# Kernel tuning notes

Hardware: AMD Instinct MI355X
Metric: run time of the kernel (lower is better)

Reference implementation:

```python
import jax, jax.numpy as jnp
import numpy as np

N, DIM, H, D = 8192, 1152, 16, 72
SEGS = 4  # equal-length image segments


def setup_inputs() -> dict:
    key = jax.random.key(0)
    ks = jax.random.split(key, 8)
    s = 0.02
    return {
        "hidden_states": jax.random.normal(ks[0], (N, DIM), jnp.float32),
        "cos": jax.random.uniform(ks[1], (N, D), jnp.float32, -1.0, 1.0),
        "sin": jax.random.uniform(ks[2], (N, D), jnp.float32, -1.0, 1.0),
        "cu_seqlens": (jnp.arange(SEGS + 1, dtype=jnp.int32) * (N // SEGS)),
        "w_qkv": jax.random.normal(ks[3], (DIM, 3 * DIM), jnp.float32) * s,
        "b_qkv": jax.random.normal(ks[4], (3 * DIM,), jnp.float32) * s,
        "w_proj": jax.random.normal(ks[5], (DIM, DIM), jnp.float32) * s,
        "b_proj": jax.random.normal(ks[6], (DIM,), jnp.float32) * s,
    }


def _rope(x, cos, sin):
    # x: [N, H, D]; cos/sin: [N, 1, D]
    half = x.shape[-1] // 2
    x1, x2 = x[..., :half], x[..., half:]
    rot = jnp.concatenate([-x2, x1], axis=-1)
    return x * cos + rot * sin


def reference(hidden_states, cos, sin, cu_seqlens, w_qkv, b_qkv, w_proj, b_proj):
    n = hidden_states.shape[0]
    qkv = (hidden_states @ w_qkv + b_qkv).reshape(n, 3, H, D)
    q, k, v = qkv[:, 0], qkv[:, 1], qkv[:, 2]
    c = cos[:, None, :]
    s = sin[:, None, :]
    q = _rope(q, c, s)
    k = _rope(k, c, s)
    # equal-length segments derived statically from cu_seqlens
    segs = int(cu_seqlens.shape[0]) - 1
    L = n // segs
    qs = q.reshape(segs, L, H, D)
    ks = k.reshape(segs, L, H, D)
    vs = v.reshape(segs, L, H, D)
    scale = D ** -0.5
    scores = jnp.einsum("slhd,smhd->shlm", qs, ks) * scale
    attn = jax.nn.softmax(scores, axis=-1)
    out = jnp.einsum("shlm,smhd->slhd", attn, vs).reshape(n, DIM)
    return out @ w_proj + b_proj
```

## Files before the change

### kernel.cpp

```cpp
#include <hip/hip_runtime.h>
#include <hip/hip_bf16.h>
#include <cstdint>
#include <cstddef>

typedef __bf16 bf16;
typedef __attribute__((ext_vector_type(8))) __bf16 bf16x8;
typedef __attribute__((ext_vector_type(4))) float f32x4;
typedef __attribute__((ext_vector_type(16))) float f32x16;
typedef __attribute__((ext_vector_type(4))) float floatx4;
typedef __attribute__((ext_vector_type(4))) unsigned short ushort4_t;
typedef __attribute__((ext_vector_type(2))) unsigned uint2_t;
typedef __attribute__((ext_vector_type(4))) unsigned uint4_t;

#define NTOK 8192
#define DIMM 1152
#define NH   16
#define HD   72
#define SEGS 4
#define SEGL 2048

__device__ __forceinline__ void gload16(const void* gsrc, void* ldst) {
  __builtin_amdgcn_global_load_lds(
      (const __attribute__((address_space(1))) void*)gsrc,
      (__attribute__((address_space(3))) void*)ldst,
      16, 0, 0);
}

__device__ __forceinline__ unsigned cvtpk(float a, float b) {
  unsigned r;
  asm volatile("v_cvt_pk_bf16_f32 %0, %1, %2" : "=v"(r) : "v"(a), "v"(b));
  return r;
}

__global__ __launch_bounds__(256) void k_cvt(const float* __restrict__ src,
                                             bf16* __restrict__ dst, int n8) {
  int i = blockIdx.x * 256 + threadIdx.x;
  if (i >= n8) return;
  const floatx4* s = (const floatx4*)src + (size_t)i * 2;
  floatx4 a = s[0], b = s[1];
  uint4_t o;
  o[0] = cvtpk(a.x, a.y);
  o[1] = cvtpk(a.z, a.w);
  o[2] = cvtpk(b.x, b.y);
  o[3] = cvtpk(b.z, b.w);
  *((uint4_t*)dst + i) = o;
}

__global__ __launch_bounds__(256) void k_twt(const float* __restrict__ src,
                                             bf16* __restrict__ dst, int R, int C) {
  __shared__ bf16 tile[64][73];
  int bc = blockIdx.x * 64, br = blockIdx.y * 64;
  int t = threadIdx.x;
#pragma unroll
  for (int i = 0; i < 16; i++) {
    int idx = i * 256 + t;
    int r = idx >> 6, c = idx & 63;
    float v = (bc + c < C) ? src[(size_t)(br + r) * C + bc + c] : 0.f;
    tile[c][r] = (bf16)v;
  }
  __syncthreads();
#pragma unroll
  for (int i = 0; i < 16; i++) {
    int idx = i * 256 + t;
    int r = idx >> 6, c = idx & 63;
    dst[(size_t)(bc + r) * R + br + c] = tile[r][c];
  }
}

template <int BM, int BN, int MI, int NI, int THREADS, bool OUT_F32>
__global__ __launch_bounds__(THREADS, 2) void k_gemmP(const bf16* __restrict__ A,
                                                      const bf16* __restrict__ Bt,
                                                      const float* __restrict__ bias,
                                                      void* __restrict__ Cout,
                                                      int M, int Nreal, int K, int gx) {
  __shared__ bf16 sA[3][BM * 32];
  __shared__ bf16 sB[3][BN * 32];
  constexpr int WN = BN / (NI * 16);
  constexpr int nA = (BM * 4) / THREADS;
  constexpr int nB = (BN * 4) / THREADS;
  constexpr int NLD = nA + nB;
  static_assert(NLD == 3 || NLD == 4, "vmcnt literal");
  const int t = threadIdx.x, wave = t >> 6, lane = t & 63;
  const int lr = lane & 15, lg = lane >> 4;
  const int nwg = gridDim.x, bid = blockIdx.x;
  const int swz = (bid & 7) * (nwg >> 3) + (bid >> 3);
  const int bx = swz % gx, by = swz / gx;
  const int m0 = by * BM, n0 = bx * BN;
  const int wr = wave / WN, wc = wave % WN;
  const int NS = K >> 5;

  f32x4 acc[MI][NI];
#pragma unroll
  for (int i = 0; i < MI; i++)
#pragma unroll
    for (int j = 0; j < NI; j++)
#pragma unroll
      for (int q = 0; q < 4; q++) acc[i][j][q] = 0.f;

  const bf16* Ab = A + (size_t)m0 * K;
  const bf16* Bb = Bt + (size_t)n0 * K;
  const int glsw = ((t & 3) ^ ((t >> 3) & 3)) * 8;
  const int rbase = t >> 2;

  auto STAGE = [&](int slot, int k0) {
#pragma unroll
    for (int p = 0; p < nA; ++p)
      gload16(Ab + (size_t)(rbase + p * (THREADS / 4)) * K + k0 + glsw,
              (char*)&sA[slot][0] + p * (THREADS * 16) + wave * 1024);
#pragma unroll
    for (int p = 0; p < nB; ++p)
      gload16(Bb + (size_t)(rbase + p * (THREADS / 4)) * K + k0 + glsw,
              (char*)&sB[slot][0] + p * (THREADS * 16) + wave * 1024);
  };

  const int swz4 = (lr >> 1) & 3;
  const int aoff = (wr * MI * 16 + lr) * 32 + ((lg ^ swz4) * 8);
  const int boff = (wc * NI * 16 + lr) * 32 + ((lg ^ swz4) * 8);

  STAGE(0, 0);
  STAGE(1, 32);

  int slot = 0;
  for (int j = 0; j < NS; ++j) {
    if (j == NS - 1) {
      asm volatile("s_waitcnt vmcnt(0)" ::: "memory");
    } else if constexpr (NLD == 3) {
      asm volatile("s_waitcnt vmcnt(3)" ::: "memory");
    } else {
      asm volatile("s_waitcnt vmcnt(4)" ::: "memory");
    }
    __builtin_amdgcn_s_barrier();
    __builtin_amdgcn_sched_barrier(0);
    bf16x8 av[MI], bv[NI];
#pragma unroll
    for (int mi = 0; mi < MI; mi++)
      av[mi] = *(const bf16x8*)&sA[slot][aoff + mi * 512];
#pragma unroll
    for (int ni = 0; ni < NI; ni++)
      bv[ni] = *(const bf16x8*)&sB[slot][boff + ni * 512];
    asm volatile("s_waitcnt lgkmcnt(0)" ::: "memory");
    __builtin_amdgcn_sched_barrier(0);
    if (j + 2 < NS) {
      int s2 = slot + 2; if (s2 >= 3) s2 -= 3;
      STAGE(s2, (j + 2) * 32);
    }
    __builtin_amdgcn_s_setprio(1);
#pragma unroll
    for (int mi = 0; mi < MI; mi++)
#pragma unroll
      for (int ni = 0; ni < NI; ni++)
        acc[mi][ni] = __builtin_amdgcn_mfma_f32_16x16x32_bf16(av[mi], bv[ni], acc[mi][ni], 0, 0, 0);
    __builtin_amdgcn_s_setprio(0);
    if (++slot == 3) slot = 0;
  }

#pragma unroll
  for (int mi = 0; mi < MI; ++mi)
#pragma unroll
    for (int ni = 0; ni < NI; ++ni) {
      int col = n0 + wc * NI * 16 + ni * 16 + lr;
      if (col < Nreal) {
        float bc_ = bias[col];
#pragma unroll
        for (int j = 0; j < 4; j++) {
          int row = m0 + wr * MI * 16 + mi * 16 + lg * 4 + j;
          float v = acc[mi][ni][j] + bc_;
          if (OUT_F32)
            ((float*)Cout)[(size_t)row * Nreal + col] = v;
          else
            ((bf16*)Cout)[(size_t)row * Nreal + col] = (bf16)v;
        }
      }
    }
}

__global__ __launch_bounds__(256) void k_rope(const bf16* __restrict__ qkv,
                                              const float* __restrict__ cs,
                                              const float* __restrict__ sn,
                                              bf16* __restrict__ Qp,
                                              bf16* __restrict__ Kp) {
  int n = blockIdx.x;
  int s = n >> 11, l = n & 2047;
  const bf16* row = qkv + (size_t)n * (3 * DIMM);
  const float* cr = cs + (size_t)n * HD;
  const float* sr = sn + (size_t)n * HD;
  const float QS = 0.17002323f;
  for (int e = threadIdx.x; e < 3072; e += 256) {
    int which = e / 1536;
    int r = e - which * 1536;
    int h = r / 96;
    int d = r - h * 96;
    float v = 0.f;
    if (d < HD) {
      int base = which * DIMM + h * HD;
      float x = (float)row[base + d];
      float o = (d < 36) ? -(float)row[base + d + 36] : (float)row[base + d - 36];
      v = x * cr[d] + o * sr[d];
      if (which == 0) v *= QS;
    }
    bf16* dst = which ? Kp : Qp;
    dst[(((size_t)(s * NH + h) * 3 + (d >> 5)) * SEGL + l) * 32 + (d & 31)] = (bf16)v;
  }
}

__global__ __launch_bounds__(256) void k_vrep(const bf16* __restrict__ qkv,
                                              bf16* __restrict__ Vt) {
  int s = blockIdx.z, h = blockIdx.y, l0 = blockIdx.x * 64;
  __shared__ bf16 tl[64][73];
  int t = threadIdx.x;
  for (int idx = t; idx < 64 * HD; idx += 256) {
    int l = idx / HD, d = idx - l * HD;
    tl[l][d] = qkv[(size_t)(s * SEGL + l0 + l) * (3 * DIMM) + 2 * DIMM + h * HD + d];
  }
  __syncthreads();
  for (int idx = t; idx < 96 * 64; idx += 256) {
    int d = idx >> 6, l = idx & 63;
    bf16 v = (d < HD) ? tl[l][d] : ((d == HD) ? (bf16)1.f : (bf16)0.f);
    Vt[((size_t)(s * NH + h) * 96 + d) * SEGL + l0 + l] = v;
  }
}

__global__ __launch_bounds__(256, 2) void k_attn(const bf16* __restrict__ Qg,
                                                 const bf16* __restrict__ Kg,
                                                 const bf16* __restrict__ Vg,
                                                 bf16* __restrict__ Oo) {
  __shared__ bf16 sK[2][3 * 64 * 32];
  __shared__ bf16 sV[2][96 * 64];
  const int t = threadIdx.x, wave = t >> 6, lane = t & 63;
  const int c = lane & 31, hi = lane >> 5;
  const int bid = blockIdx.x;
  const int g = ((bid >> 6) << 3) | (bid & 7);
  const int qt = (bid >> 3) & 7;
  const int s = g >> 4, h = g & 15, q0 = qt * 256;
  const bf16* Qb = Qg + (size_t)(s * NH + h) * 3 * SEGL * 32;
  const bf16* Kb = Kg + (size_t)(s * NH + h) * 3 * SEGL * 32;
  const bf16* Vb = Vg + (size_t)(s * NH + h) * 96 * SEGL;

  const bf16* kq[3];
  const bf16* vq[3];
#pragma unroll
  for (int i = 0; i < 3; i++) {
    int ch = wave * 3 + i;
    int kk = ch >> 2;
    int r = (ch & 3) * 16 + (lane >> 2);
    int gg = (lane & 3) ^ ((r >> 1) & 3);
    kq[i] = Kb + (size_t)kk * (SEGL * 32) + (size_t)r * 32 + gg * 8;
    int rv = ch * 8 + (lane >> 3);
    int gv = (lane & 7) ^ (rv & 7);
    vq[i] = Vb + (size_t)rv * SEGL + gv * 8;
  }

  bf16x8 Qf[2][5];
#pragma unroll
  for (int sni = 0; sni < 2; sni++)
#pragma unroll
    for (int kk = 0; kk < 5; kk++) {
      int qr = q0 + wave * 64 + sni * 32 + c;
      Qf[sni][kk] = *(const bf16x8*)&Qb[(size_t)(kk >> 1) * (SEGL * 32) +
                                        (size_t)qr * 32 + ((kk & 1) * 2 + hi) * 8];
    }

#pragma unroll
  for (int i = 0; i < 3; i++) {
    gload16(kq[i], (char*)sK[0] + (wave * 3 + i) * 1024);
    gload16(vq[i], (char*)sV[0] + (wave * 3 + i) * 1024);
    kq[i] += 2048;
    vq[i] += 64;
  }
  __syncthreads();

  f32x16 accO[3][2];
#pragma unroll
  for (int df = 0; df < 3; df++)
#pragma unroll
    for (int sni = 0; sni < 2; sni++)
#pragma unroll
      for (int r = 0; r < 16; r++) accO[df][sni][r] = 0.f;
  f32x16 ZC;
#pragma unroll
  for (int r = 0; r < 16; r++) ZC[r] = 0.f;

  int cur = 0;
  for (int tile = 0; tile < 32; ++tile) {
    if (tile + 1 < 32) {
#pragma unroll
      for (int i = 0; i < 3; i++) {
        gload16(kq[i], (char*)sK[cur ^ 1] + (wave * 3 + i) * 1024);
        gload16(vq[i], (char*)sV[cur ^ 1] + (wave * 3 + i) * 1024);
        kq[i] += 2048;
        vq[i] += 64;
      }
    }

    f32x16 S[2][2];
    __builtin_amdgcn_s_setprio(1);
#pragma unroll
    for (int kk = 0; kk < 5; kk++) {
      bf16x8 Kf[2];
#pragma unroll
      for (int smi = 0; smi < 2; smi++) {
        int kr = smi * 32 + c;
        int gg = (((kk & 1) * 2 + hi) ^ ((kr >> 1) & 3));
        Kf[smi] = *(const bf16x8*)&sK[cur][(kk >> 1) * 2048 + kr * 32 + gg * 8];
      }
#pragma unroll
      for (int smi = 0; smi < 2; smi++)
#pragma unroll
        for (int sni = 0; sni < 2; sni++)
          S[smi][sni] = __builtin_amdgcn_mfma_f32_32x32x16_bf16(
              Kf[smi], Qf[sni][kk], kk ? S[smi][sni] : ZC, 0, 0, 0);
    }
    __builtin_amdgcn_s_setprio(0);

    __builtin_amdgcn_s_setprio(1);
#pragma unroll
    for (int kk = 0; kk < 4; kk++) {
      bf16x8 Vf[3];
#pragma unroll
      for (int df = 0; df < 3; df++) {
        int dr = df * 32 + c;
        int gg = ((kk * 2 + hi) ^ (dr & 7));
        Vf[df] = *(const bf16x8*)&sV[cur][dr * 64 + gg * 8];
      }
#pragma unroll
      for (int sni = 0; sni < 2; sni++) {
        const int smi = kk >> 1;
        const int base = (kk & 1) * 8;
        unsigned u0 = cvtpk(__builtin_amdgcn_exp2f(S[smi][sni][base + 0]),
                            __builtin_amdgcn_exp2f(S[smi][sni][base + 1]));
        unsigned u1 = cvtpk(__builtin_amdgcn_exp2f(S[smi][sni][base + 2]),
                            __builtin_amdgcn_exp2f(S[smi][sni][base + 3]));
        unsigned u2 = cvtpk(__builtin_amdgcn_exp2f(S[smi][sni][base + 4]),
                            __builtin_amdgcn_exp2f(S[smi][sni][base + 5]));
        unsigned u3 = cvtpk(__builtin_amdgcn_exp2f(S[smi][sni][base + 6]),
                            __builtin_amdgcn_exp2f(S[smi][sni][base + 7]));
        asm volatile("v_permlane32_swap_b32 %0, %1" : "+v"(u0), "+v"(u2));
        asm volatile("v_permlane32_swap_b32 %0, %1" : "+v"(u1), "+v"(u3));
        union { bf16x8 v; unsigned u[4]; } pb;
        pb.u[0] = u0; pb.u[1] = u1; pb.u[2] = u2; pb.u[3] = u3;
#pragma unroll
        for (int df = 0; df < 3; df++)
          accO[df][sni] = __builtin_amdgcn_mfma_f32_32x32x16_bf16(Vf[df], pb.v, accO[df][sni], 0, 0, 0);
      }
    }
    __builtin_amdgcn_s_setprio(0);

    __syncthreads();
    cur ^= 1;
  }

#pragma unroll
  for (int sni = 0; sni < 2; sni++) {
    float lown = accO[2][sni][4];
    float lv = lown + __shfl_xor(lown, 32, 64);
    float inv = 1.f / lv;
    int token = s * SEGL + q0 + wave * 64 + sni * 32 + c;
#pragma unroll
    for (int df = 0; df < 3; df++)
#pragma unroll
      for (int rg = 0; rg < 4; rg++) {
        int d0 = df * 32 + rg * 8 + hi * 4;
        if (d0 < HD) {
          uint2_t w;
          w[0] = cvtpk(accO[df][sni][rg * 4 + 0] * inv, accO[df][sni][rg * 4 + 1] * inv);
          w[1] = cvtpk(accO[df][sni][rg * 4 + 2] * inv, accO[df][sni][rg * 4 + 3] * inv);
          *(uint2_t*)&Oo[(size_t)token * DIMM + h * HD + d0] = w;
        }
      }
  }
}

extern "C" void kernel_launch(void* const* d_in, const int* in_sizes, int n_in,
                              void* d_out, int out_size, void* d_ws, size_t ws_size,
                              hipStream_t stream) {
  (void)in_sizes; (void)n_in; (void)out_size; (void)ws_size;
  const float* hs     = (const float*)d_in[0];
  const float* cosp   = (const float*)d_in[1];
  const float* sinp   = (const float*)d_in[2];
  const float* w_qkv  = (const float*)d_in[4];
  const float* b_qkv  = (const float*)d_in[5];
  const float* w_proj = (const float*)d_in[6];
  const float* b_proj = (const float*)d_in[7];
  float* out = (float*)d_out;

  char* ws = (char*)d_ws;
  bf16* hsb    = (bf16*)(ws + 0);
  bf16* wprojT = (bf16*)(ws + 26836992);
  bf16* qkv    = (bf16*)(ws + 29491200);
  bf16* Qp     = (bf16*)(ws + 86114304);
  bf16* Kp     = (bf16*)(ws + 111280128);
  bf16* Vt     = (bf16*)(ws + 136445952);
  bf16* ao     = (bf16*)(ws + 161611776);
  bf16* wqkvT  = (bf16*)(ws + 161611776);

  k_cvt<<<4608, 256, 0, stream>>>(hs, hsb, 1179648);
  k_twt<<<dim3(56, 18), 256, 0, stream>>>(w_qkv, wqkvT, 1152, 3456);
  k_twt<<<dim3(18, 18), 256, 0, stream>>>(w_proj, wprojT, 1152, 1152);
  k_gemmP<128, 256, 4, 4, 512, false><<<896, 512, 0, stream>>>(
      hsb, wqkvT, b_qkv, (void*)qkv, 8192, 3456, 1152, 14);
  k_rope<<<8192, 256, 0, stream>>>(qkv, cosp, sinp, Qp, Kp);
  k_vrep<<<dim3(32, 16, 4), 256, 0, stream>>>(qkv, Vt);
  k_attn<<<512, 256, 0, stream>>>(Qp, Kp, Vt, ao);
  k_gemmP<128, 128, 4, 4, 256, true><<<576, 256, 0, stream>>>(
      ao, wprojT, b_proj, (void*)out, 8192, 1152, 1152, 9);
}
```

Measured before the change: 289.8 us.

## Halve attention query tile and shrink QKV GEMM tile for more occupancy

```diff
diff --git a/kernel.cpp b/kernel.cpp
--- a/kernel.cpp
+++ b/kernel.cpp
@@ -8,7 +8,6 @@
 typedef __attribute__((ext_vector_type(4))) float f32x4;
 typedef __attribute__((ext_vector_type(16))) float f32x16;
 typedef __attribute__((ext_vector_type(4))) float floatx4;
-typedef __attribute__((ext_vector_type(4))) unsigned short ushort4_t;
 typedef __attribute__((ext_vector_type(2))) unsigned uint2_t;
 typedef __attribute__((ext_vector_type(4))) unsigned uint4_t;
 
@@ -68,7 +67,7 @@
 }
 
 template <int BM, int BN, int MI, int NI, int THREADS, bool OUT_F32>
-__global__ __launch_bounds__(THREADS, 2) void k_gemmP(const bf16* __restrict__ A,
+__global__ __launch_bounds__(THREADS, 3) void k_gemmP(const bf16* __restrict__ A,
                                                       const bf16* __restrict__ Bt,
                                                       const float* __restrict__ bias,
                                                       void* __restrict__ Cout,
@@ -220,7 +219,7 @@
   }
 }
 
-__global__ __launch_bounds__(256, 2) void k_attn(const bf16* __restrict__ Qg,
+__global__ __launch_bounds__(256, 3) void k_attn(const bf16* __restrict__ Qg,
                                                  const bf16* __restrict__ Kg,
                                                  const bf16* __restrict__ Vg,
                                                  bf16* __restrict__ Oo) {
@@ -229,9 +228,9 @@
   const int t = threadIdx.x, wave = t >> 6, lane = t & 63;
   const int c = lane & 31, hi = lane >> 5;
   const int bid = blockIdx.x;
-  const int g = ((bid >> 6) << 3) | (bid & 7);
-  const int qt = (bid >> 3) & 7;
-  const int s = g >> 4, h = g & 15, q0 = qt * 256;
+  const int g = ((bid >> 7) << 3) | (bid & 7);
+  const int qt = (bid >> 3) & 15;
+  const int s = g >> 4, h = g & 15, q0 = qt * 128;
   const bf16* Qb = Qg + (size_t)(s * NH + h) * 3 * SEGL * 32;
   const bf16* Kb = Kg + (size_t)(s * NH + h) * 3 * SEGL * 32;
   const bf16* Vb = Vg + (size_t)(s * NH + h) * 96 * SEGL;
@@ -250,15 +249,13 @@
     vq[i] = Vb + (size_t)rv * SEGL + gv * 8;
   }
 
-  bf16x8 Qf[2][5];
-#pragma unroll
-  for (int sni = 0; sni < 2; sni++)
-#pragma unroll
-    for (int kk = 0; kk < 5; kk++) {
-      int qr = q0 + wave * 64 + sni * 32 + c;
-      Qf[sni][kk] = *(const bf16x8*)&Qb[(size_t)(kk >> 1) * (SEGL * 32) +
-                                        (size_t)qr * 32 + ((kk & 1) * 2 + hi) * 8];
-    }
+  bf16x8 Qf[5];
+#pragma unroll
+  for (int kk = 0; kk < 5; kk++) {
+    int qr = q0 + wave * 32 + c;
+    Qf[kk] = *(const bf16x8*)&Qb[(size_t)(kk >> 1) * (SEGL * 32) +
+                                 (size_t)qr * 32 + ((kk & 1) * 2 + hi) * 8];
+  }
 
 #pragma unroll
   for (int i = 0; i < 3; i++) {
@@ -269,13 +266,11 @@
   }
   __syncthreads();
 
-  f32x16 accO[3][2];
+  f32x16 accO[3];
 #pragma unroll
   for (int df = 0; df < 3; df++)
 #pragma unroll
-    for (int sni = 0; sni < 2; sni++)
-#pragma unroll
-      for (int r = 0; r < 16; r++) accO[df][sni][r] = 0.f;
+    for (int r = 0; r < 16; r++) accO[df][r] = 0.f;
   f32x16 ZC;
 #pragma unroll
   for (int r = 0; r < 16; r++) ZC[r] = 0.f;
@@ -292,7 +287,7 @@
       }
     }
 
-    f32x16 S[2][2];
+    f32x16 S[2];
     __builtin_amdgcn_s_setprio(1);
 #pragma unroll
     for (int kk = 0; kk < 5; kk++) {
@@ -305,10 +300,8 @@
       }
 #pragma unroll
       for (int smi = 0; smi < 2; smi++)
-#pragma unroll
-        for (int sni = 0; sni < 2; sni++)
-          S[smi][sni] = __builtin_amdgcn_mfma_f32_32x32x16_bf16(
-              Kf[smi], Qf[sni][kk], kk ? S[smi][sni] : ZC, 0, 0, 0);
+        S[smi] = __builtin_amdgcn_mfma_f32_32x32x16_bf16(
+            Kf[smi], Qf[kk], kk ? S[smi] : ZC, 0, 0, 0);
     }
     __builtin_amdgcn_s_setprio(0);
 
@@ -322,26 +315,23 @@
         int gg = ((kk * 2 + hi) ^ (dr & 7));
         Vf[df] = *(const bf16x8*)&sV[cur][dr * 64 + gg * 8];
       }
-#pragma unroll
-      for (int sni = 0; sni < 2; sni++) {
-        const int smi = kk >> 1;
-        const int base = (kk & 1) * 8;
-        unsigned u0 = cvtpk(__builtin_amdgcn_exp2f(S[smi][sni][base + 0]),
-                            __builtin_amdgcn_exp2f(S[smi][sni][base + 1]));
-        unsigned u1 = cvtpk(__builtin_amdgcn_exp2f(S[smi][sni][base + 2]),
-                            __builtin_amdgcn_exp2f(S[smi][sni][base + 3]));
-        unsigned u2 = cvtpk(__builtin_amdgcn_exp2f(S[smi][sni][base + 4]),
-                            __builtin_amdgcn_exp2f(S[smi][sni][base + 5]));
-        unsigned u3 = cvtpk(__builtin_amdgcn_exp2f(S[smi][sni][base + 6]),
-                            __builtin_amdgcn_exp2f(S[smi][sni][base + 7]));
-        asm volatile("v_permlane32_swap_b32 %0, %1" : "+v"(u0), "+v"(u2));
-        asm volatile("v_permlane32_swap_b32 %0, %1" : "+v"(u1), "+v"(u3));
-        union { bf16x8 v; unsigned u[4]; } pb;
-        pb.u[0] = u0; pb.u[1] = u1; pb.u[2] = u2; pb.u[3] = u3;
-#pragma unroll
-        for (int df = 0; df < 3; df++)
-          accO[df][sni] = __builtin_amdgcn_mfma_f32_32x32x16_bf16(Vf[df], pb.v, accO[df][sni], 0, 0, 0);
-      }
+      const int smi = kk >> 1;
+      const int base = (kk & 1) * 8;
+      unsigned u0 = cvtpk(__builtin_amdgcn_exp2f(S[smi][base + 0]),
+                          __builtin_amdgcn_exp2f(S[smi][base + 1]));
+      unsigned u1 = cvtpk(__builtin_amdgcn_exp2f(S[smi][base + 2]),
+                          __builtin_amdgcn_exp2f(S[smi][base + 3]));
+      unsigned u2 = cvtpk(__builtin_amdgcn_exp2f(S[smi][base + 4]),
+                          __builtin_amdgcn_exp2f(S[smi][base + 5]));
+      unsigned u3 = cvtpk(__builtin_amdgcn_exp2f(S[smi][base + 6]),
+                          __builtin_amdgcn_exp2f(S[smi][base + 7]));
+      asm volatile("v_permlane32_swap_b32 %0, %1" : "+v"(u0), "+v"(u2));
+      asm volatile("v_permlane32_swap_b32 %0, %1" : "+v"(u1), "+v"(u3));
+      union { bf16x8 v; unsigned u[4]; } pb;
+      pb.u[0] = u0; pb.u[1] = u1; pb.u[2] = u2; pb.u[3] = u3;
+#pragma unroll
+      for (int df = 0; df < 3; df++)
+        accO[df] = __builtin_amdgcn_mfma_f32_32x32x16_bf16(Vf[df], pb.v, accO[df], 0, 0, 0);
     }
     __builtin_amdgcn_s_setprio(0);
 
@@ -349,12 +339,11 @@
     cur ^= 1;
   }
 
-#pragma unroll
-  for (int sni = 0; sni < 2; sni++) {
-    float lown = accO[2][sni][4];
+  {
+    float lown = accO[2][4];
     float lv = lown + __shfl_xor(lown, 32, 64);
     float inv = 1.f / lv;
-    int token = s * SEGL + q0 + wave * 64 + sni * 32 + c;
+    int token = s * SEGL + q0 + wave * 32 + c;
 #pragma unroll
     for (int df = 0; df < 3; df++)
 #pragma unroll
@@ -362,8 +351,8 @@
         int d0 = df * 32 + rg * 8 + hi * 4;
         if (d0 < HD) {
           uint2_t w;
-          w[0] = cvtpk(accO[df][sni][rg * 4 + 0] * inv, accO[df][sni][rg * 4 + 1] * inv);
-          w[1] = cvtpk(accO[df][sni][rg * 4 + 2] * inv, accO[df][sni][rg * 4 + 3] * inv);
+          w[0] = cvtpk(accO[df][rg * 4 + 0] * inv, accO[df][rg * 4 + 1] * inv);
+          w[1] = cvtpk(accO[df][rg * 4 + 2] * inv, accO[df][rg * 4 + 3] * inv);
           *(uint2_t*)&Oo[(size_t)token * DIMM + h * HD + d0] = w;
         }
       }
@@ -396,11 +385,11 @@
   k_cvt<<<4608, 256, 0, stream>>>(hs, hsb, 1179648);
   k_twt<<<dim3(56, 18), 256, 0, stream>>>(w_qkv, wqkvT, 1152, 3456);
   k_twt<<<dim3(18, 18), 256, 0, stream>>>(w_proj, wprojT, 1152, 1152);
-  k_gemmP<128, 256, 4, 4, 512, false><<<896, 512, 0, stream>>>(
-      hsb, wqkvT, b_qkv, (void*)qkv, 8192, 3456, 1152, 14);
+  k_gemmP<128, 128, 4, 4, 256, false><<<1792, 256, 0, stream>>>(
+      hsb, wqkvT, b_qkv, (void*)qkv, 8192, 3456, 1152, 28);
   k_rope<<<8192, 256, 0, stream>>>(qkv, cosp, sinp, Qp, Kp);
   k_vrep<<<dim3(32, 16, 4), 256, 0, stream>>>(qkv, Vt);
-  k_attn<<<512, 256, 0, stream>>>(Qp, Kp, Vt, ao);
+  k_attn<<<1024, 256, 0, stream>>>(Qp, Kp, Vt, ao);
   k_gemmP<128, 128, 4, 4, 256, true><<<576, 256, 0, stream>>>(
       ao, wprojT, b_proj, (void*)out, 8192, 1152, 1152, 9);
 }
```

Measured after the change: 322.0 us. 1.11x slower.
